# Performance work log

Measured on AMD Instinct MI355X. Metric: run time of the kernel, lower is better.

## Reference

```python
import jax, jax.numpy as jnp
import numpy as np

B, S = 2, 2048          # sequences, tokens per sequence (equal-length varlen batch)
HK, HV = 16, 32         # key heads, value heads (GQA ratio 2)
DK = DV = 128           # head dims (asserted equal in module)
K = 4                   # causal conv kernel width
QKV = HK * DK * 2 + HV * DV  # 8192
CHUNK = 64
EPS = 1e-6


def _causal_conv1d_silu(x, w):
    # x: [B, S, QKV], w: [QKV, K] depthwise causal conv (zero history), then SiLU
    xp = jnp.pad(x, ((0, 0), (K - 1, 0), (0, 0)))
    y = xp[:, 0:S, :] * w[:, 0]
    for j in range(1, K):
        y = y + xp[:, j:j + S, :] * w[:, j]
    return jax.nn.silu(y)


def _l2norm(x):
    return x * jax.lax.rsqrt(jnp.sum(x * x, axis=-1, keepdims=True) + EPS)


def _gdn_forward(mixed_qkv, b, a, conv_weights, dt_bias, alog):
    x = mixed_qkv.reshape(B, S, QKV)
    y = _causal_conv1d_silu(x, conv_weights)
    q = _l2norm(y[..., :HK * DK].reshape(B, S, HK, DK))
    k = _l2norm(y[..., HK * DK:2 * HK * DK].reshape(B, S, HK, DK))
    v = y[..., 2 * HK * DK:].reshape(B, S, HV, DV)
    # fused_gdn_gating: g = -exp(A_log) * softplus(a + dt_bias), beta = sigmoid(b)
    g = (-jnp.exp(alog) * jax.nn.softplus(a + dt_bias)).reshape(B, S, HV)
    beta = jax.nn.sigmoid(b).reshape(B, S, HV)
    r = HV // HK  # GQA: repeat q/k heads to match value heads
    q = jnp.repeat(q, r, axis=2)
    k = jnp.repeat(k, r, axis=2)
    scale = DK ** -0.5

    def tm(t):  # [B,S,...] -> [S//CHUNK, CHUNK, B, ...] (time-major, chunked)
        tt = jnp.moveaxis(t, 1, 0)
        return tt.reshape((S // CHUNK, CHUNK) + tt.shape[1:])

    qs, ks, vs, gs, bs = tm(q), tm(k), tm(v), tm(g), tm(beta)

    def inner(St, inp):
        # St: [B,HV,DK,DV] gated delta-rule state
        qt, kt, vt, gt, bt = inp
        St = St * jnp.exp(gt)[..., None, None]
        pred = jnp.einsum('bhk,bhkv->bhv', kt, St)
        St = St + kt[..., None] * (bt[..., None] * (vt - pred))[..., None, :]
        o = jnp.einsum('bhk,bhkv->bhv', qt * scale, St)
        return St, o

    @jax.checkpoint
    def chunk_step(St, cin):
        return jax.lax.scan(inner, St, cin)

    S0 = jnp.zeros((B, HV, DK, DV), mixed_qkv.dtype)
    _, o = jax.lax.scan(chunk_step, S0, (qs, ks, vs, gs, bs))
    o = o.reshape(S, B, HV, DV)           # [S,B,HV,DV]
    return jnp.moveaxis(o, 0, 1).reshape(B * S, HV, DV)


def setup_inputs() -> dict:
    ks = jax.random.split(jax.random.key(0), 6)
    return {
        'mixed_qkv': jax.random.normal(ks[0], (B * S, QKV), jnp.float32),
        'b': jax.random.normal(ks[1], (B * S, HV), jnp.float32),
        'a': jax.random.normal(ks[2], (B * S, HV), jnp.float32),
        'conv_weights': 0.25 * jax.random.normal(ks[3], (QKV, K), jnp.float32),
        'dt_bias': jax.random.normal(ks[4], (HV,), jnp.float32),
        'alog': jax.random.normal(ks[5], (HV,), jnp.float32),
        'cu_seqlens': jnp.arange(B + 1, dtype=jnp.int32) * S,
    }


def reference(mixed_qkv, b, a, conv_weights, dt_bias, alog, cu_seqlens):
    # cu_seqlens encodes equal-length sequences [0, S, 2S]; math uses the [B,S] reshape
    return _gdn_forward(mixed_qkv, b, a, conv_weights, dt_bias, alog)
```

## Files before the change

### kernel.cpp

```cpp
#include <hip/hip_runtime.h>
#include <hip/hip_bf16.h>


#define B_    2
#define S_    2048
#define HK_   16
#define HV_   32
#define DK_   128
#define QKV_  8192
#define EPS_  1e-6f
#define SCALE_ 0.08838834764831845f
#define CH_   16
#define NCH_  (S_ / CH_)

#define AS_GLOBAL __attribute__((address_space(1)))
#define AS_LDS    __attribute__((address_space(3)))

__device__ __forceinline__ void gload16(const float* src, float* dst) {
    __builtin_amdgcn_global_load_lds((const AS_GLOBAL void*)src,
                                     (AS_LDS void*)dst, 16, 0, 0);
}
__device__ __forceinline__ void gload4(const float* src, float* dst) {
    __builtin_amdgcn_global_load_lds((const AS_GLOBAL void*)src,
                                     (AS_LDS void*)dst, 4, 0, 0);
}

__device__ __forceinline__ float red8(float x) {
    int t;
    t = __builtin_amdgcn_update_dpp(0, __float_as_int(x), 0xB1, 0xF, 0xF, true);
    x += __int_as_float(t);
    t = __builtin_amdgcn_update_dpp(0, __float_as_int(x), 0x4E, 0xF, 0xF, true);
    x += __int_as_float(t);
    t = __builtin_amdgcn_update_dpp(0, __float_as_int(x), 0x141, 0xF, 0xF, true);
    x += __int_as_float(t);
    return x;
}

__global__ __launch_bounds__(256)
void preproc_kernel(const float* __restrict__ x, const float* __restrict__ w,
                    float* __restrict__ Y)
{
    const int seg = blockIdx.x;
    const int bt0 = blockIdx.y * 4;
    const int t0  = bt0 & (S_ - 1);
    const int tid = threadIdx.x;
    const int c0  = seg * 2048 + tid * 8;

    float4 w4[8];
#pragma unroll
    for (int i = 0; i < 8; ++i)
        w4[i] = *reinterpret_cast<const float4*>(&w[(c0 + i) * 4]);

    float h0[8], h1[8], h2[8], cur[8], y[8];

#pragma unroll
    for (int i = 0; i < 8; ++i) { h0[i] = 0.f; h1[i] = 0.f; h2[i] = 0.f; }
    if (t0 >= 3) {
        const float* r0 = &x[(size_t)(bt0 - 3) * QKV_ + c0];
        const float* r1 = &x[(size_t)(bt0 - 2) * QKV_ + c0];
        const float* r2 = &x[(size_t)(bt0 - 1) * QKV_ + c0];
#pragma unroll
        for (int i4 = 0; i4 < 2; ++i4) {
            const float4 a = *reinterpret_cast<const float4*>(r0 + i4 * 4);
            const float4 b = *reinterpret_cast<const float4*>(r1 + i4 * 4);
            const float4 c = *reinterpret_cast<const float4*>(r2 + i4 * 4);
            h0[4*i4+0]=a.x; h0[4*i4+1]=a.y; h0[4*i4+2]=a.z; h0[4*i4+3]=a.w;
            h1[4*i4+0]=b.x; h1[4*i4+1]=b.y; h1[4*i4+2]=b.z; h1[4*i4+3]=b.w;
            h2[4*i4+0]=c.x; h2[4*i4+1]=c.y; h2[4*i4+2]=c.z; h2[4*i4+3]=c.w;
        }
    }

#pragma unroll
    for (int tt = 0; tt < 4; ++tt) {
        const float* rc = &x[(size_t)(bt0 + tt) * QKV_ + c0];
#pragma unroll
        for (int i4 = 0; i4 < 2; ++i4) {
            const float4 a = *reinterpret_cast<const float4*>(rc + i4 * 4);
            cur[4*i4+0]=a.x; cur[4*i4+1]=a.y; cur[4*i4+2]=a.z; cur[4*i4+3]=a.w;
        }
#pragma unroll
        for (int i = 0; i < 8; ++i) {
            float v = h0[i]*w4[i].x + h1[i]*w4[i].y + h2[i]*w4[i].z + cur[i]*w4[i].w;
            y[i] = v / (1.f + expf(-v));
        }
        if (seg < 2) {
            float s = 0.f;
#pragma unroll
            for (int i = 0; i < 8; ++i) s += y[i] * y[i];
#pragma unroll
            for (int off = 8; off >= 1; off >>= 1)
                s += __shfl_xor(s, off, 64);
            float rn = rsqrtf(s + EPS_);
            if (seg == 0) rn *= SCALE_;
#pragma unroll
            for (int i = 0; i < 8; ++i) y[i] *= rn;
        }
        float4* dst = reinterpret_cast<float4*>(&Y[(size_t)(bt0 + tt) * QKV_ + c0]);
        dst[0] = make_float4(y[0], y[1], y[2], y[3]);
        dst[1] = make_float4(y[4], y[5], y[6], y[7]);
#pragma unroll
        for (int i = 0; i < 8; ++i) { h0[i] = h1[i]; h1[i] = h2[i]; h2[i] = cur[i]; }
    }
}

__global__ __launch_bounds__(256)
void gating_kernel(const float* __restrict__ bin, const float* __restrict__ ain,
                   const float* __restrict__ dtb, const float* __restrict__ alg,
                   float2* __restrict__ GB)
{
    const int i = blockIdx.x * 256 + threadIdx.x;
    if (i >= B_ * S_ * HV_) return;
    const int h = i & (HV_ - 1);
    const float av = ain[i] + dtb[h];
    const float sp = (av > 20.f) ? av : log1pf(expf(av));
    GB[i] = make_float2(expf(-expf(alg[h]) * sp), 1.f / (1.f + expf(-bin[i])));
}

__device__ __forceinline__ void lds_load(const float* __restrict__ Kt,
                                         const float* __restrict__ Qt,
                                         const float* __restrict__ Vt,
                                         const float* __restrict__ Gt,
                                         int kh, int vloc, int sw,
                                         float (&kf)[16], float (&qf)[16],
                                         float& vv, float2& g)
{
#pragma unroll
    for (int r = 0; r < 4; ++r) {
        const int idx = r ^ sw;
        const float4 kq = *reinterpret_cast<const float4*>(Kt + kh * 16 + idx * 4);
        const float4 qq = *reinterpret_cast<const float4*>(Qt + kh * 16 + idx * 4);
        kf[4*r+0]=kq.x; kf[4*r+1]=kq.y; kf[4*r+2]=kq.z; kf[4*r+3]=kq.w;
        qf[4*r+0]=qq.x; qf[4*r+1]=qq.y; qf[4*r+2]=qq.z; qf[4*r+3]=qq.w;
    }
    vv = Vt[vloc];
    g  = *reinterpret_cast<const float2*>(Gt);
}

__device__ __forceinline__ void step_tok(float (&S)[16],
                                         const float (&kf)[16], const float (&qf)[16],
                                         float vv, float2 g, int kh,
                                         float* __restrict__ optr)
{
    const float eg = g.x, bt = g.y;
    float p0 = 0.f, p1 = 0.f, p2 = 0.f, p3 = 0.f;
#pragma unroll
    for (int j = 0; j < 16; j += 4) {
        p0 += kf[j+0] * S[j+0];
        p1 += kf[j+1] * S[j+1];
        p2 += kf[j+2] * S[j+2];
        p3 += kf[j+3] * S[j+3];
    }
    float pred = red8((p0 + p1) + (p2 + p3));
    const float delta = bt * (vv - pred * eg);

    float o0 = 0.f, o1 = 0.f, o2 = 0.f, o3 = 0.f;
#pragma unroll
    for (int j = 0; j < 16; j += 4) {
        float s0 = fmaf(eg, S[j+0], kf[j+0] * delta); S[j+0] = s0; o0 += qf[j+0] * s0;
        float s1 = fmaf(eg, S[j+1], kf[j+1] * delta); S[j+1] = s1; o1 += qf[j+1] * s1;
        float s2 = fmaf(eg, S[j+2], kf[j+2] * delta); S[j+2] = s2; o2 += qf[j+2] * s2;
        float s3 = fmaf(eg, S[j+3], kf[j+3] * delta); S[j+3] = s3; o3 += qf[j+3] * s3;
    }
    float o = red8((o0 + o1) + (o2 + o3));
    if (kh == 0) *optr = o;
}

__global__ __launch_bounds__(64, 1)
void recur_kernel(const float* __restrict__ Y, const float2* __restrict__ GB,
                  float* __restrict__ out)
{
    const int h    = blockIdx.x;
    const int b    = blockIdx.y;
    const int vs   = blockIdx.z;
    const int hk   = h >> 1;
    const int lane = threadIdx.x;
    const int kh   = lane & 7;
    const int vloc = lane >> 3;
    const int sw   = kh >> 1;

    const int qoff0 = hk * DK_;
    const int koff0 = 2048 + hk * DK_;
    const int voff0 = 4096 + h * DK_ + vs * 8;

    __shared__ __align__(16) float Ksm[2][CH_][128];
    __shared__ __align__(16) float Qsm[2][CH_][128];
    __shared__ __align__(16) float Vsm[2][CH_ * 8];
    __shared__ __align__(16) float Gsm[2][64];

    const float* rowBase = Y + (size_t)(b * S_) * QKV_;
    const float* gflat   = (const float*)(GB + (size_t)(b * S_) * HV_ + h);
    float* obase = out + ((size_t)(b * S_) * HV_ + h) * (size_t)DK_ + vs * 8 + vloc;

    const int tk = lane >> 5;
    const int gr = lane & 31;

    auto issue_chunk = [&](int t0, int bsel) {
#pragma unroll
        for (int i = 0; i < 8; ++i)
            gload16(rowBase + (size_t)(t0 + 2 * i + tk) * QKV_ + koff0 + gr * 4,
                    &Ksm[bsel][2 * i][0]);
#pragma unroll
        for (int i = 0; i < 8; ++i)
            gload16(rowBase + (size_t)(t0 + 2 * i + tk) * QKV_ + qoff0 + gr * 4,
                    &Qsm[bsel][2 * i][0]);
#pragma unroll
        for (int i = 0; i < 2; ++i)
            gload4(rowBase + (size_t)(t0 + i * 8 + (lane >> 3)) * QKV_
                           + voff0 + (lane & 7),
                   &Vsm[bsel][i * 64]);
        gload4(gflat + (size_t)(t0 + ((lane >> 1) & 15)) * (HV_ * 2) + (lane & 1),
               &Gsm[bsel][0]);
    };

    float S[16];
#pragma unroll
    for (int j = 0; j < 16; ++j) S[j] = 0.f;

    issue_chunk(0, 0);
    issue_chunk(CH_, 1);
    asm volatile("s_waitcnt vmcnt(19)" ::: "memory");

    float kA[16], qA[16], vA, kB[16], qB[16], vB;
    float2 gA, gB2;

    for (int c = 0; c < NCH_; ++c) {
        const int bsel = c & 1;
        const int t0   = c * CH_;
        const float (*Kc)[128] = Ksm[bsel];
        const float (*Qc)[128] = Qsm[bsel];
        const float* Vc = Vsm[bsel];
        const float* Gc = Gsm[bsel];

        lds_load(Kc[0], Qc[0], Vc + 0, Gc + 0, kh, vloc, sw, kA, qA, vA, gA);
        lds_load(Kc[1], Qc[1], Vc + 8, Gc + 2, kh, vloc, sw, kB, qB, vB, gB2);
#pragma unroll
        for (int tt = 0; tt < CH_; tt += 2) {
            step_tok(S, kA, qA, vA, gA, kh,
                     obase + (size_t)(t0 + tt) * (HV_ * DK_));
            if (tt + 2 < CH_)
                lds_load(Kc[tt + 2], Qc[tt + 2], Vc + (tt + 2) * 8, Gc + (tt + 2) * 2,
                         kh, vloc, sw, kA, qA, vA, gA);
            __builtin_amdgcn_sched_barrier(0);
            step_tok(S, kB, qB, vB, gB2, kh,
                     obase + (size_t)(t0 + tt + 1) * (HV_ * DK_));
            if (tt + 3 < CH_)
                lds_load(Kc[tt + 3], Qc[tt + 3], Vc + (tt + 3) * 8, Gc + (tt + 3) * 2,
                         kh, vloc, sw, kB, qB, vB, gB2);
        }

        const int tn = (c + 2 < NCH_) ? (c + 2) * CH_ : (NCH_ - 1) * CH_;
        issue_chunk(tn, bsel);
        asm volatile("s_waitcnt vmcnt(35)" ::: "memory");
    }
}

__global__ __launch_bounds__(128)
void gdn_prefill_fallback(const float* __restrict__ xqkv, const float* __restrict__ bin,
                          const float* __restrict__ ain, const float* __restrict__ wconv,
                          const float* __restrict__ dtb, const float* __restrict__ alg,
                          float* __restrict__ out)
{
    const int h = blockIdx.x, b = blockIdx.y;
    const int hk = h >> 1;
    const int tid = threadIdx.x, lane = tid & 63, wid = tid >> 6;
    __shared__ __align__(16) float ks[DK_];
    __shared__ __align__(16) float qs[DK_];
    __shared__ float redq[2], redk[2];
    const int qc = hk * DK_ + tid, kc = HK_ * DK_ + hk * DK_ + tid,
              vc = 2 * HK_ * DK_ + h * DK_ + tid;
    float wq[4], wk[4], wv[4];
#pragma unroll
    for (int j = 0; j < 4; ++j) {
        wq[j] = wconv[qc*4+j]; wk[j] = wconv[kc*4+j]; wv[j] = wconv[vc*4+j];
    }
    const float nea = -expf(alg[h]), dbi = dtb[h];
    float hq0=0,hq1=0,hq2=0,hk0=0,hk1=0,hk2=0,hv0=0,hv1=0,hv2=0;
    float Sr[DK_];
#pragma unroll
    for (int k = 0; k < DK_; ++k) Sr[k] = 0.f;
    const size_t row0 = (size_t)b * S_;
    for (int t = 0; t < S_; ++t) {
        const size_t row = row0 + t, xb = row * QKV_;
        const float xq = xqkv[xb+qc], xk = xqkv[xb+kc], xv = xqkv[xb+vc];
        float yq = hq0*wq[0]+hq1*wq[1]+hq2*wq[2]+xq*wq[3];
        float yk = hk0*wk[0]+hk1*wk[1]+hk2*wk[2]+xk*wk[3];
        float yv = hv0*wv[0]+hv1*wv[1]+hv2*wv[2]+xv*wv[3];
        hq0=hq1;hq1=hq2;hq2=xq; hk0=hk1;hk1=hk2;hk2=xk; hv0=hv1;hv1=hv2;hv2=xv;
        yq = yq/(1.f+expf(-yq)); yk = yk/(1.f+expf(-yk)); yv = yv/(1.f+expf(-yv));
        float sq = yq*yq, sk = yk*yk;
#pragma unroll
        for (int off = 32; off >= 1; off >>= 1) {
            sq += __shfl_xor(sq, off, 64); sk += __shfl_xor(sk, off, 64);
        }
        if (lane == 0) { redq[wid] = sq; redk[wid] = sk; }
        __syncthreads();
        const float qn = yq * rsqrtf(redq[0]+redq[1]+EPS_) * SCALE_;
        const float kn = yk * rsqrtf(redk[0]+redk[1]+EPS_);
        ks[tid] = kn; qs[tid] = qn;
        const size_t rab = row * HV_ + h;
        const float av = ain[rab] + dbi;
        const float sp = (av > 20.f) ? av : log1pf(expf(av));
        const float eg = expf(nea * sp);
        const float beta = 1.f/(1.f+expf(-bin[rab]));
        __syncthreads();
        float pred = 0.f;
#pragma unroll
        for (int k4 = 0; k4 < DK_/4; ++k4) {
            const float4 kv = *reinterpret_cast<const float4*>(&ks[k4*4]);
            float s;
            s = Sr[4*k4+0]*eg; Sr[4*k4+0]=s; pred += kv.x*s;
            s = Sr[4*k4+1]*eg; Sr[4*k4+1]=s; pred += kv.y*s;
            s = Sr[4*k4+2]*eg; Sr[4*k4+2]=s; pred += kv.z*s;
            s = Sr[4*k4+3]*eg; Sr[4*k4+3]=s; pred += kv.w*s;
        }
        const float delta = beta * (yv - pred);
        float o = 0.f;
#pragma unroll
        for (int k4 = 0; k4 < DK_/4; ++k4) {
            const float4 kv = *reinterpret_cast<const float4*>(&ks[k4*4]);
            const float4 qv = *reinterpret_cast<const float4*>(&qs[k4*4]);
            float s;
            s = Sr[4*k4+0]+kv.x*delta; Sr[4*k4+0]=s; o += qv.x*s;
            s = Sr[4*k4+1]+kv.y*delta; Sr[4*k4+1]=s; o += qv.y*s;
            s = Sr[4*k4+2]+kv.z*delta; Sr[4*k4+2]=s; o += qv.z*s;
            s = Sr[4*k4+3]+kv.w*delta; Sr[4*k4+3]=s; o += qv.w*s;
        }
        out[rab * DK_ + tid] = o;
    }
}

extern "C" void kernel_launch(void* const* d_in, const int* in_sizes, int n_in,
                              void* d_out, int out_size, void* d_ws, size_t ws_size,
                              hipStream_t stream) {
    const float* xqkv  = (const float*)d_in[0];
    const float* bin   = (const float*)d_in[1];
    const float* ain   = (const float*)d_in[2];
    const float* wconv = (const float*)d_in[3];
    const float* dtb   = (const float*)d_in[4];
    const float* alg   = (const float*)d_in[5];
    float* out = (float*)d_out;

    const size_t Y_BYTES = (size_t)B_ * S_ * QKV_ * 4;
    const size_t G_BYTES = (size_t)B_ * S_ * HV_ * 8;
    const size_t NEEDED  = Y_BYTES + G_BYTES;

    if (ws_size >= NEEDED) {
        float*  Y  = (float*)d_ws;
        float2* GB = (float2*)((char*)d_ws + Y_BYTES);

        preproc_kernel<<<dim3(4, B_ * S_ / 4), 256, 0, stream>>>(xqkv, wconv, Y);
        gating_kernel<<<dim3((B_ * S_ * HV_ + 255) / 256), 256, 0, stream>>>(
            bin, ain, dtb, alg, GB);
        recur_kernel<<<dim3(HV_, B_, 16), 64, 0, stream>>>(Y, GB, out);
    } else {
        gdn_prefill_fallback<<<dim3(HV_, B_), 128, 0, stream>>>(
            xqkv, bin, ain, wconv, dtb, alg, out);
    }
}
```

Measured before the change: 821.0 us.

## Process token pairs algebraically to halve serial cross-lane reductions in recurrence

Replaces the per-token delta-rule step with a two-token step. It computes eight dot products (k0·S, k1·S, k1·k0, q·S, q·k) up front, reduces all eight together, and derives both outputs and the combined state update in closed form. This removes the serial dependency between token t's state update and token t+1's reductions, so the red8 shuffle chains can overlap. The cost is more FMAs per pair, double the register footprint for prefetched k/q vectors, and slightly different float rounding.

```diff
diff --git a/kernel.cpp b/kernel.cpp
--- a/kernel.cpp
+++ b/kernel.cpp
@@ -116,13 +116,12 @@
     GB[i] = make_float2(expf(-expf(alg[h]) * sp), 1.f / (1.f + expf(-bin[i])));
 }
 
-__device__ __forceinline__ void lds_load(const float* __restrict__ Kt,
-                                         const float* __restrict__ Qt,
-                                         const float* __restrict__ Vt,
-                                         const float* __restrict__ Gt,
-                                         int kh, int vloc, int sw,
-                                         float (&kf)[16], float (&qf)[16],
-                                         float& vv, float2& g)
+__device__ __forceinline__ void lds_load_kqv(const float* __restrict__ Kt,
+                                             const float* __restrict__ Qt,
+                                             const float* __restrict__ Vt,
+                                             int kh, int vloc, int sw,
+                                             float (&kf)[16], float (&qf)[16],
+                                             float& vv)
 {
 #pragma unroll
     for (int r = 0; r < 4; ++r) {
@@ -133,36 +132,43 @@
         qf[4*r+0]=qq.x; qf[4*r+1]=qq.y; qf[4*r+2]=qq.z; qf[4*r+3]=qq.w;
     }
     vv = Vt[vloc];
-    g  = *reinterpret_cast<const float2*>(Gt);
-}
-
-__device__ __forceinline__ void step_tok(float (&S)[16],
-                                         const float (&kf)[16], const float (&qf)[16],
-                                         float vv, float2 g, int kh,
-                                         float* __restrict__ optr)
-{
-    const float eg = g.x, bt = g.y;
-    float p0 = 0.f, p1 = 0.f, p2 = 0.f, p3 = 0.f;
-#pragma unroll
-    for (int j = 0; j < 16; j += 4) {
-        p0 += kf[j+0] * S[j+0];
-        p1 += kf[j+1] * S[j+1];
-        p2 += kf[j+2] * S[j+2];
-        p3 += kf[j+3] * S[j+3];
-    }
-    float pred = red8((p0 + p1) + (p2 + p3));
-    const float delta = bt * (vv - pred * eg);
-
-    float o0 = 0.f, o1 = 0.f, o2 = 0.f, o3 = 0.f;
-#pragma unroll
-    for (int j = 0; j < 16; j += 4) {
-        float s0 = fmaf(eg, S[j+0], kf[j+0] * delta); S[j+0] = s0; o0 += qf[j+0] * s0;
-        float s1 = fmaf(eg, S[j+1], kf[j+1] * delta); S[j+1] = s1; o1 += qf[j+1] * s1;
-        float s2 = fmaf(eg, S[j+2], kf[j+2] * delta); S[j+2] = s2; o2 += qf[j+2] * s2;
-        float s3 = fmaf(eg, S[j+3], kf[j+3] * delta); S[j+3] = s3; o3 += qf[j+3] * s3;
-    }
-    float o = red8((o0 + o1) + (o2 + o3));
-    if (kh == 0) *optr = o;
+}
+
+__device__ __forceinline__ void step_pair(float (&S)[16],
+    const float (&k0)[16], const float (&q0)[16], float v0,
+    const float (&k1)[16], const float (&q1)[16], float v1,
+    float4 g,
+    int kh, float* __restrict__ o0p, float* __restrict__ o1p)
+{
+    float a0 = 0.f, a1 = 0.f, cc = 0.f, u0 = 0.f,
+          u1 = 0.f, w00 = 0.f, w10 = 0.f, w11 = 0.f;
+#pragma unroll
+    for (int j = 0; j < 16; ++j) {
+        a0  += k0[j] * S[j];
+        a1  += k1[j] * S[j];
+        cc  += k1[j] * k0[j];
+        u0  += q0[j] * S[j];
+        u1  += q1[j] * S[j];
+        w00 += q0[j] * k0[j];
+        w10 += q1[j] * k0[j];
+        w11 += q1[j] * k1[j];
+    }
+    a0 = red8(a0);  a1 = red8(a1);  cc = red8(cc);  u0 = red8(u0);
+    u1 = red8(u1);  w00 = red8(w00); w10 = red8(w10); w11 = red8(w11);
+
+    const float eg0 = g.x, b0 = g.y, eg1 = g.z, b1 = g.w;
+    const float d0   = b0 * (v0 - eg0 * a0);
+    const float eg01 = eg0 * eg1;
+    const float p1   = fmaf(eg1 * cc, d0, eg01 * a1);
+    const float d1   = b1 * (v1 - p1);
+    const float o0   = fmaf(w00, d0, eg0 * u0);
+    const float o1   = fmaf(w11, d1, fmaf(eg1 * w10, d0, eg01 * u1));
+    const float bb   = eg1 * d0;
+#pragma unroll
+    for (int j = 0; j < 16; ++j)
+        S[j] = fmaf(eg01, S[j], fmaf(bb, k0[j], d1 * k1[j]));
+
+    if (kh == 0) { *o0p = o0; *o1p = o1; }
 }
 
 __global__ __launch_bounds__(64, 1)
@@ -220,8 +226,9 @@
     issue_chunk(CH_, 1);
     asm volatile("s_waitcnt vmcnt(19)" ::: "memory");
 
-    float kA[16], qA[16], vA, kB[16], qB[16], vB;
-    float2 gA, gB2;
+    float k0A[16], q0A[16], k1A[16], q1A[16], v0A, v1A;
+    float k0B[16], q0B[16], k1B[16], q1B[16], v0B, v1B;
+    float4 gA, gB4;
 
     for (int c = 0; c < NCH_; ++c) {
         const int bsel = c & 1;
@@ -231,21 +238,38 @@
         const float* Vc = Vsm[bsel];
         const float* Gc = Gsm[bsel];
 
-        lds_load(Kc[0], Qc[0], Vc + 0, Gc + 0, kh, vloc, sw, kA, qA, vA, gA);
-        lds_load(Kc[1], Qc[1], Vc + 8, Gc + 2, kh, vloc, sw, kB, qB, vB, gB2);
-#pragma unroll
-        for (int tt = 0; tt < CH_; tt += 2) {
-            step_tok(S, kA, qA, vA, gA, kh,
-                     obase + (size_t)(t0 + tt) * (HV_ * DK_));
-            if (tt + 2 < CH_)
-                lds_load(Kc[tt + 2], Qc[tt + 2], Vc + (tt + 2) * 8, Gc + (tt + 2) * 2,
-                         kh, vloc, sw, kA, qA, vA, gA);
+        lds_load_kqv(Kc[0], Qc[0], Vc + 0,  kh, vloc, sw, k0A, q0A, v0A);
+        lds_load_kqv(Kc[1], Qc[1], Vc + 8,  kh, vloc, sw, k1A, q1A, v1A);
+        gA = *reinterpret_cast<const float4*>(Gc + 0);
+        lds_load_kqv(Kc[2], Qc[2], Vc + 16, kh, vloc, sw, k0B, q0B, v0B);
+        lds_load_kqv(Kc[3], Qc[3], Vc + 24, kh, vloc, sw, k1B, q1B, v1B);
+        gB4 = *reinterpret_cast<const float4*>(Gc + 4);
+
+#pragma unroll
+        for (int pp = 0; pp < CH_ / 2; pp += 2) {
+            step_pair(S, k0A, q0A, v0A, k1A, q1A, v1A, gA, kh,
+                      obase + (size_t)(t0 + 2 * pp)     * (HV_ * DK_),
+                      obase + (size_t)(t0 + 2 * pp + 1) * (HV_ * DK_));
+            if (pp + 2 < CH_ / 2) {
+                const int ta = 2 * (pp + 2);
+                lds_load_kqv(Kc[ta],     Qc[ta],     Vc + ta * 8,
+                             kh, vloc, sw, k0A, q0A, v0A);
+                lds_load_kqv(Kc[ta + 1], Qc[ta + 1], Vc + (ta + 1) * 8,
+                             kh, vloc, sw, k1A, q1A, v1A);
+                gA = *reinterpret_cast<const float4*>(Gc + 2 * ta);
+            }
             __builtin_amdgcn_sched_barrier(0);
-            step_tok(S, kB, qB, vB, gB2, kh,
-                     obase + (size_t)(t0 + tt + 1) * (HV_ * DK_));
-            if (tt + 3 < CH_)
-                lds_load(Kc[tt + 3], Qc[tt + 3], Vc + (tt + 3) * 8, Gc + (tt + 3) * 2,
-                         kh, vloc, sw, kB, qB, vB, gB2);
+            step_pair(S, k0B, q0B, v0B, k1B, q1B, v1B, gB4, kh,
+                      obase + (size_t)(t0 + 2 * pp + 2) * (HV_ * DK_),
+                      obase + (size_t)(t0 + 2 * pp + 3) * (HV_ * DK_));
+            if (pp + 3 < CH_ / 2) {
+                const int tb = 2 * (pp + 3);
+                lds_load_kqv(Kc[tb],     Qc[tb],     Vc + tb * 8,
+                             kh, vloc, sw, k0B, q0B, v0B);
+                lds_load_kqv(Kc[tb + 1], Qc[tb + 1], Vc + (tb + 1) * 8,
+                             kh, vloc, sw, k1B, q1B, v1B);
+                gB4 = *reinterpret_cast<const float4*>(Gc + 2 * tb);
+            }
         }
 
         const int tn = (c + 2 < NCH_) ? (c + 2) * CH_ : (NCH_ - 1) * CH_;
```

Measured after the change: 827.2 us. About the same (+0.8%).

## Process tokens in groups of four using precomputed intra-group k·k and q·k dots

Applied to the files above, without the earlier changes.

Adds a dot_kernel that precomputes, for each group of four tokens, the pairwise k·k and q·k dot products per key head. The recurrence now advances the state four tokens at a time. It computes all q·S and k·S reductions against the group-start state at once and resolves the intra-group delta dependencies with the precomputed dots, then applies one fused state update. This removes three of every four serial reduce-update round trips on the critical path, at the cost of an extra kernel, more registers, and a changed floating-point evaluation order.

```diff
diff --git a/kernel.cpp b/kernel.cpp
--- a/kernel.cpp
+++ b/kernel.cpp
@@ -116,58 +116,63 @@
     GB[i] = make_float2(expf(-expf(alg[h]) * sp), 1.f / (1.f + expf(-bin[i])));
 }
 
-__device__ __forceinline__ void lds_load(const float* __restrict__ Kt,
-                                         const float* __restrict__ Qt,
-                                         const float* __restrict__ Vt,
-                                         const float* __restrict__ Gt,
-                                         int kh, int vloc, int sw,
-                                         float (&kf)[16], float (&qf)[16],
-                                         float& vv, float2& g)
+__global__ __launch_bounds__(256)
+void dot_kernel(const float* __restrict__ Y, float4* __restrict__ CD4)
 {
-#pragma unroll
-    for (int r = 0; r < 4; ++r) {
-        const int idx = r ^ sw;
-        const float4 kq = *reinterpret_cast<const float4*>(Kt + kh * 16 + idx * 4);
-        const float4 qq = *reinterpret_cast<const float4*>(Qt + kh * 16 + idx * 4);
-        kf[4*r+0]=kq.x; kf[4*r+1]=kq.y; kf[4*r+2]=kq.z; kf[4*r+3]=kq.w;
-        qf[4*r+0]=qq.x; qf[4*r+1]=qq.y; qf[4*r+2]=qq.z; qf[4*r+3]=qq.w;
-    }
-    vv = Vt[vloc];
-    g  = *reinterpret_cast<const float2*>(Gt);
-}
-
-__device__ __forceinline__ void step_tok(float (&S)[16],
-                                         const float (&kf)[16], const float (&qf)[16],
-                                         float vv, float2 g, int kh,
-                                         float* __restrict__ optr)
-{
-    const float eg = g.x, bt = g.y;
-    float p0 = 0.f, p1 = 0.f, p2 = 0.f, p3 = 0.f;
-#pragma unroll
-    for (int j = 0; j < 16; j += 4) {
-        p0 += kf[j+0] * S[j+0];
-        p1 += kf[j+1] * S[j+1];
-        p2 += kf[j+2] * S[j+2];
-        p3 += kf[j+3] * S[j+3];
-    }
-    float pred = red8((p0 + p1) + (p2 + p3));
-    const float delta = bt * (vv - pred * eg);
-
-    float o0 = 0.f, o1 = 0.f, o2 = 0.f, o3 = 0.f;
-#pragma unroll
-    for (int j = 0; j < 16; j += 4) {
-        float s0 = fmaf(eg, S[j+0], kf[j+0] * delta); S[j+0] = s0; o0 += qf[j+0] * s0;
-        float s1 = fmaf(eg, S[j+1], kf[j+1] * delta); S[j+1] = s1; o1 += qf[j+1] * s1;
-        float s2 = fmaf(eg, S[j+2], kf[j+2] * delta); S[j+2] = s2; o2 += qf[j+2] * s2;
-        float s3 = fmaf(eg, S[j+3], kf[j+3] * delta); S[j+3] = s3; o3 += qf[j+3] * s3;
-    }
-    float o = red8((o0 + o1) + (o2 + o3));
-    if (kh == 0) *optr = o;
+    const int lane = threadIdx.x & 63;
+    const int i    = blockIdx.x * 4 + (threadIdx.x >> 6);
+    const int grp  = i & 511;
+    const int bh   = i >> 9;
+    const int hk   = bh & (HK_ - 1);
+    const int b    = bh >> 4;
+    const int ch   = lane * 2;
+    const size_t r0 = (size_t)(b * S_ + grp * 4) * QKV_;
+    const int koff = 2048 + hk * DK_ + ch;
+    const int qoff = hk * DK_ + ch;
+
+    float2 k0 = *reinterpret_cast<const float2*>(Y + r0 + 0 * QKV_ + koff);
+    float2 k1 = *reinterpret_cast<const float2*>(Y + r0 + 1 * QKV_ + koff);
+    float2 k2 = *reinterpret_cast<const float2*>(Y + r0 + 2 * QKV_ + koff);
+    float2 k3 = *reinterpret_cast<const float2*>(Y + r0 + 3 * QKV_ + koff);
+    float2 q0 = *reinterpret_cast<const float2*>(Y + r0 + 0 * QKV_ + qoff);
+    float2 q1 = *reinterpret_cast<const float2*>(Y + r0 + 1 * QKV_ + qoff);
+    float2 q2 = *reinterpret_cast<const float2*>(Y + r0 + 2 * QKV_ + qoff);
+    float2 q3 = *reinterpret_cast<const float2*>(Y + r0 + 3 * QKV_ + qoff);
+
+    float d[16];
+    d[0]  = k1.x*k0.x + k1.y*k0.y;
+    d[1]  = k2.x*k0.x + k2.y*k0.y;
+    d[2]  = k2.x*k1.x + k2.y*k1.y;
+    d[3]  = k3.x*k0.x + k3.y*k0.y;
+    d[4]  = k3.x*k1.x + k3.y*k1.y;
+    d[5]  = k3.x*k2.x + k3.y*k2.y;
+    d[6]  = q0.x*k0.x + q0.y*k0.y;
+    d[7]  = q1.x*k0.x + q1.y*k0.y;
+    d[8]  = q1.x*k1.x + q1.y*k1.y;
+    d[9]  = q2.x*k0.x + q2.y*k0.y;
+    d[10] = q2.x*k1.x + q2.y*k1.y;
+    d[11] = q2.x*k2.x + q2.y*k2.y;
+    d[12] = q3.x*k0.x + q3.y*k0.y;
+    d[13] = q3.x*k1.x + q3.y*k1.y;
+    d[14] = q3.x*k2.x + q3.y*k2.y;
+    d[15] = q3.x*k3.x + q3.y*k3.y;
+#pragma unroll
+    for (int t = 0; t < 16; ++t)
+#pragma unroll
+        for (int off = 32; off >= 1; off >>= 1)
+            d[t] += __shfl_xor(d[t], off, 64);
+
+    if (lane == 0) {
+        CD4[(size_t)i * 4 + 0] = make_float4(d[0],  d[1],  d[2],  d[3]);
+        CD4[(size_t)i * 4 + 1] = make_float4(d[4],  d[5],  d[6],  d[7]);
+        CD4[(size_t)i * 4 + 2] = make_float4(d[8],  d[9],  d[10], d[11]);
+        CD4[(size_t)i * 4 + 3] = make_float4(d[12], d[13], d[14], d[15]);
+    }
 }
 
 __global__ __launch_bounds__(64, 1)
 void recur_kernel(const float* __restrict__ Y, const float2* __restrict__ GB,
-                  float* __restrict__ out)
+                  const float* __restrict__ CDg, float* __restrict__ out)
 {
     const int h    = blockIdx.x;
     const int b    = blockIdx.y;
@@ -186,9 +191,11 @@
     __shared__ __align__(16) float Qsm[2][CH_][128];
     __shared__ __align__(16) float Vsm[2][CH_ * 8];
     __shared__ __align__(16) float Gsm[2][64];
+    __shared__ __align__(16) float CDsm[2][64];
 
     const float* rowBase = Y + (size_t)(b * S_) * QKV_;
     const float* gflat   = (const float*)(GB + (size_t)(b * S_) * HV_ + h);
+    const float* cdflat  = CDg + (size_t)(b * HK_ + hk) * 512 * 16;
     float* obase = out + ((size_t)(b * S_) * HV_ + h) * (size_t)DK_ + vs * 8 + vloc;
 
     const int tk = lane >> 5;
@@ -210,6 +217,7 @@
                    &Vsm[bsel][i * 64]);
         gload4(gflat + (size_t)(t0 + ((lane >> 1) & 15)) * (HV_ * 2) + (lane & 1),
                &Gsm[bsel][0]);
+        gload4(cdflat + (size_t)(t0 / 4) * 16 + lane, &CDsm[bsel][0]);
     };
 
     float S[16];
@@ -218,39 +226,131 @@
 
     issue_chunk(0, 0);
     issue_chunk(CH_, 1);
-    asm volatile("s_waitcnt vmcnt(19)" ::: "memory");
-
-    float kA[16], qA[16], vA, kB[16], qB[16], vB;
-    float2 gA, gB2;
+    asm volatile("s_waitcnt vmcnt(20)" ::: "memory");
+
+    float kf[4][16], qf[4][16];
+#pragma unroll
+    for (int i = 0; i < 4; ++i)
+#pragma unroll
+        for (int r = 0; r < 4; ++r) {
+            const int idx = r ^ sw;
+            const float4 kq = *reinterpret_cast<const float4*>(&Ksm[0][i][kh*16 + idx*4]);
+            const float4 qq = *reinterpret_cast<const float4*>(&Qsm[0][i][kh*16 + idx*4]);
+            kf[i][4*r+0]=kq.x; kf[i][4*r+1]=kq.y; kf[i][4*r+2]=kq.z; kf[i][4*r+3]=kq.w;
+            qf[i][4*r+0]=qq.x; qf[i][4*r+1]=qq.y; qf[i][4*r+2]=qq.z; qf[i][4*r+3]=qq.w;
+        }
 
     for (int c = 0; c < NCH_; ++c) {
         const int bsel = c & 1;
         const int t0   = c * CH_;
         const float (*Kc)[128] = Ksm[bsel];
         const float (*Qc)[128] = Qsm[bsel];
-        const float* Vc = Vsm[bsel];
-        const float* Gc = Gsm[bsel];
-
-        lds_load(Kc[0], Qc[0], Vc + 0, Gc + 0, kh, vloc, sw, kA, qA, vA, gA);
-        lds_load(Kc[1], Qc[1], Vc + 8, Gc + 2, kh, vloc, sw, kB, qB, vB, gB2);
-#pragma unroll
-        for (int tt = 0; tt < CH_; tt += 2) {
-            step_tok(S, kA, qA, vA, gA, kh,
-                     obase + (size_t)(t0 + tt) * (HV_ * DK_));
-            if (tt + 2 < CH_)
-                lds_load(Kc[tt + 2], Qc[tt + 2], Vc + (tt + 2) * 8, Gc + (tt + 2) * 2,
-                         kh, vloc, sw, kA, qA, vA, gA);
+        const float (*Kn)[128] = Ksm[bsel ^ 1];
+        const float (*Qn)[128] = Qsm[bsel ^ 1];
+        const float* Vc  = Vsm[bsel];
+        const float* Gc  = Gsm[bsel];
+        const float* CDc = CDsm[bsel];
+
+#pragma unroll
+        for (int g = 0; g < 4; ++g) {
+            const float4 ga  = *reinterpret_cast<const float4*>(Gc + 8*g);
+            const float4 gbv = *reinterpret_cast<const float4*>(Gc + 8*g + 4);
+            const float4 cd0 = *reinterpret_cast<const float4*>(CDc + 16*g);
+            const float4 cd1 = *reinterpret_cast<const float4*>(CDc + 16*g + 4);
+            const float4 cd2 = *reinterpret_cast<const float4*>(CDc + 16*g + 8);
+            const float4 cd3 = *reinterpret_cast<const float4*>(CDc + 16*g + 12);
+            const float v0 = Vc[(4*g+0)*8 + vloc], v1 = Vc[(4*g+1)*8 + vloc];
+            const float v2 = Vc[(4*g+2)*8 + vloc], v3 = Vc[(4*g+3)*8 + vloc];
+
+            float u0=0.f,u1=0.f,u2=0.f,u3=0.f;
+#pragma unroll
+            for (int j = 0; j < 16; ++j) {
+                u0 += qf[0][j]*S[j]; u1 += qf[1][j]*S[j];
+                u2 += qf[2][j]*S[j]; u3 += qf[3][j]*S[j];
+            }
+            float a0=0.f,a1=0.f,a2=0.f,a3=0.f;
+#pragma unroll
+            for (int j = 0; j < 16; ++j) {
+                a0 += kf[0][j]*S[j]; a1 += kf[1][j]*S[j];
+                a2 += kf[2][j]*S[j]; a3 += kf[3][j]*S[j];
+            }
+            u0=red8(u0); u1=red8(u1); u2=red8(u2); u3=red8(u3);
+            a0=red8(a0); a1=red8(a1); a2=red8(a2); a3=red8(a3);
+
+            if (g == 3) {
+                asm volatile("s_waitcnt lgkmcnt(0)" ::: "memory");
+                const int tn = (c + 2 < NCH_) ? (c + 2) * CH_ : (NCH_ - 1) * CH_;
+                issue_chunk(tn, bsel);
+                asm volatile("s_waitcnt vmcnt(32)" ::: "memory");
+            }
+            {
+                const float (*Qs)[128] = (g == 3) ? Qn : Qc;
+                const int gb = (g == 3) ? 0 : (g + 1) * 4;
+#pragma unroll
+                for (int i = 0; i < 4; ++i)
+#pragma unroll
+                    for (int r = 0; r < 4; ++r) {
+                        const int idx = r ^ sw;
+                        const float4 qq = *reinterpret_cast<const float4*>(
+                            &Qs[gb + i][kh*16 + idx*4]);
+                        qf[i][4*r+0]=qq.x; qf[i][4*r+1]=qq.y;
+                        qf[i][4*r+2]=qq.z; qf[i][4*r+3]=qq.w;
+                    }
+            }
             __builtin_amdgcn_sched_barrier(0);
-            step_tok(S, kB, qB, vB, gB2, kh,
-                     obase + (size_t)(t0 + tt + 1) * (HV_ * DK_));
-            if (tt + 3 < CH_)
-                lds_load(Kc[tt + 3], Qc[tt + 3], Vc + (tt + 3) * 8, Gc + (tt + 3) * 2,
-                         kh, vloc, sw, kB, qB, vB, gB2);
-        }
-
-        const int tn = (c + 2 < NCH_) ? (c + 2) * CH_ : (NCH_ - 1) * CH_;
-        issue_chunk(tn, bsel);
-        asm volatile("s_waitcnt vmcnt(35)" ::: "memory");
+
+            const float e0=ga.x, bb0=ga.y, e1=ga.z, bb1=ga.w;
+            const float e2=gbv.x, bb2=gbv.y, e3=gbv.z, bb3=gbv.w;
+            const float c10=cd0.x, c20=cd0.y, c21=cd0.z, c30=cd0.w;
+            const float c31=cd1.x, c32=cd1.y, w00=cd1.z, w10=cd1.w;
+            const float w11=cd2.x, w20=cd2.y, w21=cd2.z, w22=cd2.w;
+            const float w30=cd3.x, w31=cd3.y, w32=cd3.z, w33=cd3.w;
+
+            const float e01 = e0*e1, e12 = e1*e2, e23 = e2*e3;
+            const float e012 = e01*e2, e123 = e12*e3, e0123 = e012*e3;
+            const float d0 = bb0 * (v0 - e0*a0);
+            const float d1 = bb1 * (v1 - e01*a1 - e1*c10*d0);
+            const float d2 = bb2 * (v2 - e012*a2 - e12*c20*d0 - e2*c21*d1);
+            const float d3 = bb3 * (v3 - e0123*a3 - e123*c30*d0 - e23*c31*d1
+                                       - e3*c32*d2);
+            const float o0 = fmaf(w00, d0, e0*u0);
+            const float o1 = fmaf(w11, d1, fmaf(e1*w10, d0, e01*u1));
+            const float o2 = fmaf(w22, d2, fmaf(e2*w21, d1,
+                              fmaf(e12*w20, d0, e012*u2)));
+            const float o3 = fmaf(w33, d3, fmaf(e3*w32, d2,
+                              fmaf(e23*w31, d1, fmaf(e123*w30, d0, e0123*u3))));
+            if (kh == 0) {
+                float* op = obase + (size_t)(t0 + 4*g) * (HV_ * DK_);
+                op[0]                 = o0;
+                op[1 * HV_ * DK_]     = o1;
+                op[2 * HV_ * DK_]     = o2;
+                op[3 * HV_ * DK_]     = o3;
+            }
+
+            const float f0 = e123*d0, f1 = e23*d1, f2 = e3*d2;
+#pragma unroll
+            for (int j = 0; j < 16; ++j)
+                S[j] = fmaf(e0123, S[j],
+                        fmaf(f0, kf[0][j],
+                          fmaf(f1, kf[1][j],
+                            fmaf(f2, kf[2][j], d3*kf[3][j]))));
+
+            {
+                const float (*Ks)[128] = (g == 3) ? Kn : Kc;
+                const int gb = (g == 3) ? 0 : (g + 1) * 4;
+#pragma unroll
+                for (int i = 0; i < 4; ++i)
+#pragma unroll
+                    for (int r = 0; r < 4; ++r) {
+                        const int idx = r ^ sw;
+                        const float4 kq = *reinterpret_cast<const float4*>(
+                            &Ks[gb + i][kh*16 + idx*4]);
+                        kf[i][4*r+0]=kq.x; kf[i][4*r+1]=kq.y;
+                        kf[i][4*r+2]=kq.z; kf[i][4*r+3]=kq.w;
+                    }
+            }
+            __builtin_amdgcn_sched_barrier(0);
+        }
     }
 }
 
@@ -340,18 +440,22 @@
     const float* alg   = (const float*)d_in[5];
     float* out = (float*)d_out;
 
-    const size_t Y_BYTES = (size_t)B_ * S_ * QKV_ * 4;
-    const size_t G_BYTES = (size_t)B_ * S_ * HV_ * 8;
-    const size_t NEEDED  = Y_BYTES + G_BYTES;
+    const size_t Y_BYTES  = (size_t)B_ * S_ * QKV_ * 4;
+    const size_t G_BYTES  = (size_t)B_ * S_ * HV_ * 8;
+    const size_t CD_BYTES = (size_t)B_ * HK_ * 512 * 16 * 4;
+    const size_t NEEDED   = Y_BYTES + G_BYTES + CD_BYTES;
 
     if (ws_size >= NEEDED) {
         float*  Y  = (float*)d_ws;
         float2* GB = (float2*)((char*)d_ws + Y_BYTES);
+        float*  CD = (float*)((char*)d_ws + Y_BYTES + G_BYTES);
 
         preproc_kernel<<<dim3(4, B_ * S_ / 4), 256, 0, stream>>>(xqkv, wconv, Y);
         gating_kernel<<<dim3((B_ * S_ * HV_ + 255) / 256), 256, 0, stream>>>(
             bin, ain, dtb, alg, GB);
-        recur_kernel<<<dim3(HV_, B_, 16), 64, 0, stream>>>(Y, GB, out);
+        dot_kernel<<<dim3(B_ * HK_ * 512 / 4), 256, 0, stream>>>(
+            Y, (float4*)CD);
+        recur_kernel<<<dim3(HV_, B_, 16), 64, 0, stream>>>(Y, GB, CD, out);
     } else {
         gdn_prefill_fallback<<<dim3(HV_, B_), 128, 0, stream>>>(
             xqkv, bin, ain, wconv, dtb, alg, out);
```

Result: faster. 690.6 us (-15.9%).
